# Optimization experiments

Measured on AMD Instinct MI355X. Metric: run time of the kernel, lower is better.

The kernel has to match this reference:

```python
import jax, jax.numpy as jnp
import numpy as np

D = 256   # input_size
H = 512   # hidden_size
A = 4     # alpha_dim
K = 2 * A * A  # output values per input dim (binary=False -> 2 params)


def _masks():
    # MADE sequential-ordering masks, per DART.create_masks
    in_deg = np.arange(D)
    hid_deg = np.arange(H) % (D - 1)
    out_deg = np.arange(D) - 1  # arange(D) % D - 1
    m0 = (hid_deg[:, None] >= in_deg[None, :]).astype(np.float32)   # [H, D]
    mh = (hid_deg[:, None] >= hid_deg[None, :]).astype(np.float32)  # [H, H]
    ml = (out_deg[:, None] >= hid_deg[None, :]).astype(np.float32)  # [D, H]
    # repeat(1, K).view(-1, H): each output-dim row repeated K consecutive times
    ml = np.repeat(ml, K, axis=0)                                    # [D*K, H]
    return jnp.asarray(m0), jnp.asarray(mh), jnp.asarray(ml)


def setup_inputs() -> dict:
    key = jax.random.key(0)
    ks = jax.random.split(key, 10)
    B = 1024
    x = jax.random.normal(ks[0], (B, D), dtype=jnp.float32)
    def lin(k, out_dim, in_dim):
        s = 1.0 / np.sqrt(in_dim)
        kw, kb = jax.random.split(k)
        W = jax.random.uniform(kw, (out_dim, in_dim), jnp.float32, -s, s)
        b = jax.random.uniform(kb, (out_dim,), jnp.float32, -s, s)
        return W, b
    W0, b0 = lin(ks[1], H, D)
    W1, b1 = lin(ks[2], H, H)
    W2, b2 = lin(ks[3], H, H)
    Wout, bout = lin(ks[4], D * K, H)
    # unnormalized_log_p_alpha initialized to log(1/A)
    ulpa = jnp.full((1, D - 1, 1, A), -np.log(A), dtype=jnp.float32)
    return {"x": x, "W0": W0, "b0": b0, "W1": W1, "b1": b1,
            "W2": W2, "b2": b2, "Wout": Wout, "bout": bout, "ulpa": ulpa}


def reference(x, W0, b0, W1, b1, W2, b2, Wout, bout, ulpa):
    m0, mh, ml = _masks()
    B = x.shape[0]
    # masked MLP (MADE)
    h = jax.nn.relu(x @ (m0 * W0).T + b0)
    h = jax.nn.relu(h @ (mh * W1).T + b1)
    h = jax.nn.relu(h @ (mh * W2).T + b2)
    theta = (h @ (ml * Wout).T + bout).reshape(B, D, 2, A, A)
    mu = theta[:, :, 0]                      # [B, D, A, A]
    std = jnp.exp(theta[:, :, 1]) + 0.01     # [B, D, A, A]
    xe = x[:, :, None, None]
    # Normal log-prob
    log_px = -0.5 * jnp.square((xe - mu) / std) - jnp.log(std) - 0.5 * jnp.log(2.0 * jnp.pi)
    # normalized log p(alpha): [1, D-1, 1, A]
    lpa = jax.nn.log_softmax(ulpa, axis=-1)
    joint = log_px[:, :-1] + lpa             # [B, D-1, A, A]
    first = joint[:, 0, 0:1]                 # [B, 1, A]
    inner = jnp.swapaxes(joint[:, 1:], 0, 1)  # [D-2, B, A, A]
    # HMM-style forward recursion: stable log-domain chain matmul via scan
    def step(carry, m):
        # carry: [B, 1, A]; m: [B, A, A]
        new = jax.nn.logsumexp(carry[:, :, :, None] + m[:, None, :, :], axis=-2)
        return new, None
    carry, _ = jax.lax.scan(step, first, inner)
    last = log_px[:, -1, :, 0:1]             # [B, A, 1]
    log_p = jax.nn.logsumexp(carry[:, :, :, None] + last[:, None, :, :], axis=-2)  # [B,1,1]
    return log_p, theta
```

## Files before the change

### kernel.cpp

```cpp
#include <hip/hip_runtime.h>
#include <math.h>

#define Bsz 1024
#define Dd  256
#define Hh  512
#define NOUT 8192

typedef __attribute__((ext_vector_type(8))) short bf8_t;
typedef __attribute__((ext_vector_type(4))) float f4_t;

__device__ inline ushort f2b(float f) {
  union { float f; unsigned u; } c; c.f = f;
  unsigned r = c.u + 0x7fffu + ((c.u >> 16) & 1u);
  return (ushort)(r >> 16);
}

__device__ inline void async16(const ushort* g, ushort* l) {
  __builtin_amdgcn_global_load_lds((const __attribute__((address_space(1))) void*)g,
                                   (__attribute__((address_space(3))) void*)l, 16, 0, 0);
}

__device__ inline int mod255(int v) {
  if (v >= 510) return v - 510;
  if (v >= 255) return v - 255;
  return v;
}

__global__ __launch_bounds__(256) void prep(
    const float* __restrict__ x,  const float* __restrict__ W0,
    const float* __restrict__ W1, const float* __restrict__ W2,
    const float* __restrict__ Wout, const float* __restrict__ ulpa,
    ushort* __restrict__ xb, ushort* __restrict__ w0b, ushort* __restrict__ w1b,
    ushort* __restrict__ w2b, ushort* __restrict__ woutb,
    float* __restrict__ lpa)
{
  const int blk = blockIdx.x, tid = threadIdx.x;
  if (blk == 2496) {
    if (tid < Dd - 1) {
      float v0 = ulpa[tid * 4 + 0], v1 = ulpa[tid * 4 + 1];
      float v2 = ulpa[tid * 4 + 2], v3 = ulpa[tid * 4 + 3];
      float m = fmaxf(fmaxf(v0, v1), fmaxf(v2, v3));
      float s = __expf(v0 - m) + __expf(v1 - m) + __expf(v2 - m) + __expf(v3 - m);
      float l = m + __logf(s);
      lpa[tid * 4 + 0] = v0 - l;
      lpa[tid * 4 + 1] = v1 - l;
      lpa[tid * 4 + 2] = v2 - l;
      lpa[tid * 4 + 3] = v3 - l;
    }
    return;
  }
  const float* src; ushort* dst; int lb, mode;
  if (blk < 128)      { src = x;    dst = xb;    lb = blk;       mode = 0; }
  else if (blk < 192) { src = W0;   dst = w0b;   lb = blk - 128; mode = 1; }
  else if (blk < 320) { src = W1;   dst = w1b;   lb = blk - 192; mode = 2; }
  else if (blk < 448) { src = W2;   dst = w2b;   lb = blk - 320; mode = 2; }
  else                { src = Wout; dst = woutb; lb = blk - 448; mode = 3; }

  const int e = lb * 2048 + tid * 8;
  float4 v0 = *(const float4*)(src + e);
  float4 v1 = *(const float4*)(src + e + 4);
  float vv[8] = {v0.x, v0.y, v0.z, v0.w, v1.x, v1.y, v1.z, v1.w};
  ushort u[8];
  if (mode == 0) {
#pragma unroll
    for (int i = 0; i < 8; i++) u[i] = f2b(vv[i]);
  } else if (mode == 1) {
    int n = e >> 8, k0 = e & 255, nd = mod255(n);
#pragma unroll
    for (int i = 0; i < 8; i++) u[i] = (nd >= k0 + i) ? f2b(vv[i]) : (ushort)0;
  } else if (mode == 2) {
    int n = e >> 9, k0 = e & 511, nd = mod255(n);
#pragma unroll
    for (int i = 0; i < 8; i++) u[i] = (nd >= mod255(k0 + i)) ? f2b(vv[i]) : (ushort)0;
  } else {
    int n = e >> 9, k0 = e & 511, nd = (n >> 5) - 1;
#pragma unroll
    for (int i = 0; i < 8; i++) u[i] = (nd >= mod255(k0 + i)) ? f2b(vv[i]) : (ushort)0;
  }
  *(ushort4*)(dst + e)     = *(ushort4*)&u[0];
  *(ushort4*)(dst + e + 4) = *(ushort4*)&u[4];
}

template<int KD>
__global__ __launch_bounds__(256) void gemm_s(
    const ushort* __restrict__ A, const ushort* __restrict__ W,
    const float* __restrict__ bias, ushort* __restrict__ Ch)
{
  __shared__ ushort As[64 * 64];
  __shared__ ushort Bs[32 * 64];
  const int tid = threadIdx.x, lane = tid & 63, wave = tid >> 6;
  const int row0 = blockIdx.y * 64, col0 = blockIdx.x * 32;
  const int fm = lane & 15, qq = lane >> 4;
  const int srow = lane >> 3, qslot = lane & 7;

  f4_t acc[2];
  acc[0] = (f4_t){0.f, 0.f, 0.f, 0.f};
  acc[1] = (f4_t){0.f, 0.f, 0.f, 0.f};

  for (int kt = 0; kt < KD; kt += 64) {
#pragma unroll
    for (int a = 0; a < 2; a++) {
      int rb = wave * 16 + a * 8;
      int r = rb + srow;
      int q = (qslot - r) & 7;
      async16(A + (size_t)(row0 + r) * KD + kt + q * 8, &As[rb * 64]);
    }
    {
      int rb = wave * 8;
      int r = rb + srow;
      int q = (qslot - r) & 7;
      async16(W + (size_t)(col0 + r) * KD + kt + q * 8, &Bs[rb * 64]);
    }
    __syncthreads();
#pragma unroll
    for (int t = 0; t < 2; t++) {
      int ra = wave * 16 + fm;
      int slota = ((t * 4 + qq) + ra) & 7;
      bf8_t af = *(const bf8_t*)&As[ra * 64 + slota * 8];
#pragma unroll
      for (int j = 0; j < 2; j++) {
        int rb = j * 16 + fm;
        int slot = ((t * 4 + qq) + rb) & 7;
        bf8_t bf = *(const bf8_t*)&Bs[rb * 64 + slot * 8];
        acc[j] = __builtin_amdgcn_mfma_f32_16x16x32_bf16(af, bf, acc[j], 0, 0, 0);
      }
    }
    __syncthreads();
  }

#pragma unroll
  for (int j = 0; j < 2; j++) {
    int col = col0 + j * 16 + fm;
    float bv = bias[col];
    int rbase = row0 + wave * 16 + qq * 4;
#pragma unroll
    for (int r = 0; r < 4; r++) {
      float t = fmaxf(acc[j][r] + bv, 0.0f);
      Ch[(size_t)(rbase + r) * Hh + col] = f2b(t);
    }
  }
}

__global__ __launch_bounds__(256) void gemm_big(
    const ushort* __restrict__ A, const ushort* __restrict__ W,
    const float* __restrict__ bias, float* __restrict__ Cf,
    int M, int N, int Kd)
{
  __shared__ ushort As[128 * 64];
  __shared__ ushort Bs[128 * 64];
  const int tid = threadIdx.x, lane = tid & 63, wave = tid >> 6;
  const int waveM = wave >> 1, waveN = wave & 1;
  const int row0 = blockIdx.y * 128, col0 = blockIdx.x * 128;
  const int fm = lane & 15, qq = lane >> 4;
  const int srow = lane >> 3, qslot = lane & 7;

  f4_t acc[4][4];
#pragma unroll
  for (int i = 0; i < 4; i++)
#pragma unroll
    for (int j = 0; j < 4; j++) acc[i][j] = (f4_t){0.f, 0.f, 0.f, 0.f};

  for (int kt = 0; kt < Kd; kt += 64) {
#pragma unroll
    for (int p = 0; p < 4; p++) {
      int rb = p * 32 + wave * 8;
      int r = rb + srow;
      int q = (qslot - r) & 7;
      async16(A + (size_t)(row0 + r) * Kd + kt + q * 8, &As[rb * 64]);
    }
#pragma unroll
    for (int p = 0; p < 4; p++) {
      int rb = p * 32 + wave * 8;
      int r = rb + srow;
      int q = (qslot - r) & 7;
      async16(W + (size_t)(col0 + r) * Kd + kt + q * 8, &Bs[rb * 64]);
    }
    __syncthreads();
#pragma unroll
    for (int t = 0; t < 2; t++) {
      bf8_t af[4], bf[4];
#pragma unroll
      for (int i = 0; i < 4; i++) {
        int r = waveM * 64 + i * 16 + fm;
        int slot = ((t * 4 + qq) + r) & 7;
        af[i] = *(const bf8_t*)&As[r * 64 + slot * 8];
      }
#pragma unroll
      for (int j = 0; j < 4; j++) {
        int r = waveN * 64 + j * 16 + fm;
        int slot = ((t * 4 + qq) + r) & 7;
        bf[j] = *(const bf8_t*)&Bs[r * 64 + slot * 8];
      }
#pragma unroll
      for (int i = 0; i < 4; i++)
#pragma unroll
        for (int j = 0; j < 4; j++)
          acc[i][j] = __builtin_amdgcn_mfma_f32_16x16x32_bf16(af[i], bf[j], acc[i][j], 0, 0, 0);
    }
    __syncthreads();
  }

#pragma unroll
  for (int j = 0; j < 4; j++) {
    int col = col0 + waveN * 64 + j * 16 + fm;
    float bv = bias[col];
#pragma unroll
    for (int i = 0; i < 4; i++) {
      int rbase = row0 + waveM * 64 + i * 16 + qq * 4;
#pragma unroll
      for (int r = 0; r < 4; r++)
        Cf[(size_t)(rbase + r) * N + col] = acc[i][j][r] + bv;
    }
  }
}

__global__ __launch_bounds__(256) void chain2(
    const float* __restrict__ x, const float* __restrict__ theta,
    const float* __restrict__ lpa, float* __restrict__ logp)
{
  const int b = blockIdx.x;
  const int tid = threadIdx.x;
  const int seg = tid >> 4, e = tid & 15;
  const int i = e >> 2, jj = e & 3;
  const int base = (tid & 63) & ~15;
  const float C0 = 0.91893853320467274178f;
  const float* th = theta + (size_t)b * NOUT;
  const float* xb = x + (size_t)b * Dd;
  __shared__ float Ts[16][16];

  const int d0 = 1 + seg * 16;
  const int d1 = min(d0 + 16, Dd - 1);

  auto stepm = [&](int d) -> float {
    float mu = th[d * 32 + e];
    float ls = th[d * 32 + 16 + e];
    float s  = __expf(ls) + 0.01f;
    float z  = (xb[d] - mu) * __builtin_amdgcn_rcpf(s);
    return -0.5f * z * z - __logf(s) - C0 + lpa[d * 4 + jj];
  };

  float T = stepm(d0);
  for (int d = d0 + 1; d < d1; d++) {
    float m_ = stepm(d);
    float v0 = __shfl(T, base + i * 4 + 0) + __shfl(m_, base + 0 * 4 + jj);
    float v1 = __shfl(T, base + i * 4 + 1) + __shfl(m_, base + 1 * 4 + jj);
    float v2 = __shfl(T, base + i * 4 + 2) + __shfl(m_, base + 2 * 4 + jj);
    float v3 = __shfl(T, base + i * 4 + 3) + __shfl(m_, base + 3 * 4 + jj);
    float mx = fmaxf(fmaxf(v0, v1), fmaxf(v2, v3));
    float s  = __expf(v0 - mx) + __expf(v1 - mx) + __expf(v2 - mx) + __expf(v3 - mx);
    T = mx + __logf(s);
  }
  Ts[seg][e] = T;
  __syncthreads();

  if (tid < 4) {
    const int j = tid;
    float mu = th[j], ls = th[16 + j];
    float s = __expf(ls) + 0.01f;
    float z = (xb[0] - mu) * __builtin_amdgcn_rcpf(s);
    float carry = -0.5f * z * z - __logf(s) - C0 + lpa[j];
#pragma unroll 1
    for (int sg = 0; sg < 16; sg++) {
      float c0 = __shfl(carry, 0);
      float c1 = __shfl(carry, 1);
      float c2 = __shfl(carry, 2);
      float c3 = __shfl(carry, 3);
      float v0 = c0 + Ts[sg][0 * 4 + j];
      float v1 = c1 + Ts[sg][1 * 4 + j];
      float v2 = c2 + Ts[sg][2 * 4 + j];
      float v3 = c3 + Ts[sg][3 * 4 + j];
      float mx = fmaxf(fmaxf(v0, v1), fmaxf(v2, v3));
      float ss = __expf(v0 - mx) + __expf(v1 - mx) + __expf(v2 - mx) + __expf(v3 - mx);
      carry = mx + __logf(ss);
    }
    float mu2 = th[255 * 32 + j * 4], ls2 = th[255 * 32 + 16 + j * 4];
    float s2 = __expf(ls2) + 0.01f;
    float z2 = (xb[255] - mu2) * __builtin_amdgcn_rcpf(s2);
    float v = carry - 0.5f * z2 * z2 - __logf(s2) - C0;
    float mx = fmaxf(v, __shfl_xor(v, 1));
    mx = fmaxf(mx, __shfl_xor(mx, 2));
    float ee = __expf(v - mx);
    ee += __shfl_xor(ee, 1);
    ee += __shfl_xor(ee, 2);
    if (j == 0) logp[b] = mx + __logf(ee);
  }
}

extern "C" void kernel_launch(void* const* d_in, const int* in_sizes, int n_in,
                              void* d_out, int out_size, void* d_ws, size_t ws_size,
                              hipStream_t stream)
{
  const float* x    = (const float*)d_in[0];
  const float* W0   = (const float*)d_in[1];
  const float* b0   = (const float*)d_in[2];
  const float* W1   = (const float*)d_in[3];
  const float* b1   = (const float*)d_in[4];
  const float* W2   = (const float*)d_in[5];
  const float* b2   = (const float*)d_in[6];
  const float* Wout = (const float*)d_in[7];
  const float* bout = (const float*)d_in[8];
  const float* ulpa = (const float*)d_in[9];

  float* out   = (float*)d_out;
  float* logp  = out;
  float* theta = out + Bsz;

  ushort* ws    = (ushort*)d_ws;
  ushort* xb    = ws;
  ushort* w0b   = xb + 262144;
  ushort* w1b   = w0b + 131072;
  ushort* w2b   = w1b + 262144;
  ushort* woutb = w2b + 262144;
  ushort* h0    = woutb + 4194304;
  ushort* h1    = h0 + 524288;
  ushort* h2    = h1 + 524288;
  float*  lpa   = (float*)(h2 + 524288);

  prep<<<2497, 256, 0, stream>>>(x, W0, W1, W2, Wout, ulpa,
                                 xb, w0b, w1b, w2b, woutb, lpa);
  gemm_s<Dd><<<dim3(16, 16), 256, 0, stream>>>(xb, w0b, b0, h0);
  gemm_s<Hh><<<dim3(16, 16), 256, 0, stream>>>(h0, w1b, b1, h1);
  gemm_s<Hh><<<dim3(16, 16), 256, 0, stream>>>(h1, w2b, b2, h2);
  gemm_big<<<dim3(NOUT / 128, Bsz / 128), 256, 0, stream>>>(h2, woutb, bout, theta, Bsz, NOUT, Hh);
  chain2<<<Bsz, 256, 0, stream>>>(x, theta, lpa, logp);
}
```

Before: 139.5 us.

## Multi-buffer GEMM tile loads and parallelize chain reduction with a tree

The small GEMMs now use a triple-buffered LDS pipeline and the output GEMM a double-buffered one. Async global-to-LDS loads for the next tiles are issued before computing the current tile, with explicit vmcnt waits and barriers in place of __syncthreads. The chain kernel moves to 512 threads: it stages each row's theta, x and log p(alpha) into padded shared memory, runs shorter 8-step segments, and combines the 32 segment matrices with a log-depth tree of log-semiring matrix products instead of a serial 16-step loop. The GEMM changes aim to hide global load latency at the cost of more LDS per block, and the chain changes aim to shorten its serial dependency chain.

```diff
diff --git a/kernel.cpp b/kernel.cpp
--- a/kernel.cpp
+++ b/kernel.cpp
@@ -86,8 +86,9 @@
     const ushort* __restrict__ A, const ushort* __restrict__ W,
     const float* __restrict__ bias, ushort* __restrict__ Ch)
 {
-  __shared__ ushort As[64 * 64];
-  __shared__ ushort Bs[32 * 64];
+  constexpr int NT = KD / 64;
+  __shared__ ushort As[3][64 * 64];
+  __shared__ ushort Bs[3][32 * 64];
   const int tid = threadIdx.x, lane = tid & 63, wave = tid >> 6;
   const int row0 = blockIdx.y * 64, col0 = blockIdx.x * 32;
   const int fm = lane & 15, qq = lane >> 4;
@@ -97,35 +98,47 @@
   acc[0] = (f4_t){0.f, 0.f, 0.f, 0.f};
   acc[1] = (f4_t){0.f, 0.f, 0.f, 0.f};
 
-  for (int kt = 0; kt < KD; kt += 64) {
+  auto stage = [&](int buf, int kt) {
 #pragma unroll
     for (int a = 0; a < 2; a++) {
       int rb = wave * 16 + a * 8;
       int r = rb + srow;
       int q = (qslot - r) & 7;
-      async16(A + (size_t)(row0 + r) * KD + kt + q * 8, &As[rb * 64]);
+      async16(A + (size_t)(row0 + r) * KD + kt + q * 8, &As[buf][rb * 64]);
     }
     {
       int rb = wave * 8;
       int r = rb + srow;
       int q = (qslot - r) & 7;
-      async16(W + (size_t)(col0 + r) * KD + kt + q * 8, &Bs[rb * 64]);
-    }
-    __syncthreads();
+      async16(W + (size_t)(col0 + r) * KD + kt + q * 8, &Bs[buf][rb * 64]);
+    }
+  };
+
+  stage(0, 0);
+  stage(1, 64);
+
+#pragma unroll
+  for (int i = 0; i < NT; i++) {
+    if (i + 1 < NT) asm volatile("s_waitcnt vmcnt(3)" ::: "memory");
+    else            asm volatile("s_waitcnt vmcnt(0)" ::: "memory");
+    __builtin_amdgcn_s_barrier();
+    asm volatile("" ::: "memory");
+    if (i + 2 < NT) stage((i + 2) % 3, (i + 2) * 64);
+    const int buf = i % 3;
 #pragma unroll
     for (int t = 0; t < 2; t++) {
       int ra = wave * 16 + fm;
       int slota = ((t * 4 + qq) + ra) & 7;
-      bf8_t af = *(const bf8_t*)&As[ra * 64 + slota * 8];
+      bf8_t af = *(const bf8_t*)&As[buf][ra * 64 + slota * 8];
 #pragma unroll
       for (int j = 0; j < 2; j++) {
         int rb = j * 16 + fm;
         int slot = ((t * 4 + qq) + rb) & 7;
-        bf8_t bf = *(const bf8_t*)&Bs[rb * 64 + slot * 8];
+        bf8_t bf = *(const bf8_t*)&Bs[buf][rb * 64 + slot * 8];
         acc[j] = __builtin_amdgcn_mfma_f32_16x16x32_bf16(af, bf, acc[j], 0, 0, 0);
       }
     }
-    __syncthreads();
+    asm volatile("s_waitcnt lgkmcnt(0)" ::: "memory");
   }
 
 #pragma unroll
@@ -146,8 +159,8 @@
     const float* __restrict__ bias, float* __restrict__ Cf,
     int M, int N, int Kd)
 {
-  __shared__ ushort As[128 * 64];
-  __shared__ ushort Bs[128 * 64];
+  __shared__ ushort As[2][128 * 64];
+  __shared__ ushort Bs[2][128 * 64];
   const int tid = threadIdx.x, lane = tid & 63, wave = tid >> 6;
   const int waveM = wave >> 1, waveN = wave & 1;
   const int row0 = blockIdx.y * 128, col0 = blockIdx.x * 128;
@@ -160,22 +173,30 @@
 #pragma unroll
     for (int j = 0; j < 4; j++) acc[i][j] = (f4_t){0.f, 0.f, 0.f, 0.f};
 
-  for (int kt = 0; kt < Kd; kt += 64) {
+  auto stage = [&](int buf, int kt) {
 #pragma unroll
     for (int p = 0; p < 4; p++) {
       int rb = p * 32 + wave * 8;
       int r = rb + srow;
       int q = (qslot - r) & 7;
-      async16(A + (size_t)(row0 + r) * Kd + kt + q * 8, &As[rb * 64]);
+      async16(A + (size_t)(row0 + r) * Kd + kt + q * 8, &As[buf][rb * 64]);
     }
 #pragma unroll
     for (int p = 0; p < 4; p++) {
       int rb = p * 32 + wave * 8;
       int r = rb + srow;
       int q = (qslot - r) & 7;
-      async16(W + (size_t)(col0 + r) * Kd + kt + q * 8, &Bs[rb * 64]);
-    }
-    __syncthreads();
+      async16(W + (size_t)(col0 + r) * Kd + kt + q * 8, &Bs[buf][rb * 64]);
+    }
+  };
+
+  stage(0, 0);
+  int cur = 0;
+  for (int kt = 0; kt < Kd; kt += 64) {
+    asm volatile("s_waitcnt vmcnt(0)" ::: "memory");
+    __builtin_amdgcn_s_barrier();
+    asm volatile("" ::: "memory");
+    if (kt + 64 < Kd) stage(cur ^ 1, kt + 64);
 #pragma unroll
     for (int t = 0; t < 2; t++) {
       bf8_t af[4], bf[4];
@@ -183,13 +204,13 @@
       for (int i = 0; i < 4; i++) {
         int r = waveM * 64 + i * 16 + fm;
         int slot = ((t * 4 + qq) + r) & 7;
-        af[i] = *(const bf8_t*)&As[r * 64 + slot * 8];
+        af[i] = *(const bf8_t*)&As[cur][r * 64 + slot * 8];
       }
 #pragma unroll
       for (int j = 0; j < 4; j++) {
         int r = waveN * 64 + j * 16 + fm;
         int slot = ((t * 4 + qq) + r) & 7;
-        bf[j] = *(const bf8_t*)&Bs[r * 64 + slot * 8];
+        bf[j] = *(const bf8_t*)&Bs[cur][r * 64 + slot * 8];
       }
 #pragma unroll
       for (int i = 0; i < 4; i++)
@@ -197,7 +218,8 @@
         for (int j = 0; j < 4; j++)
           acc[i][j] = __builtin_amdgcn_mfma_f32_16x16x32_bf16(af[i], bf[j], acc[i][j], 0, 0, 0);
     }
-    __syncthreads();
+    asm volatile("s_waitcnt lgkmcnt(0)" ::: "memory");
+    cur ^= 1;
   }
 
 #pragma unroll
@@ -214,75 +236,106 @@
   }
 }
 
-__global__ __launch_bounds__(256) void chain2(
+__global__ __launch_bounds__(512) void chain2(
     const float* __restrict__ x, const float* __restrict__ theta,
     const float* __restrict__ lpa, float* __restrict__ logp)
 {
+  __shared__ float ths[256 * 33];
+  __shared__ float xs[256];
+  __shared__ float lps[255 * 5];
+  __shared__ float TA[32][16];
+  __shared__ float TB[16][16];
+
   const int b = blockIdx.x;
   const int tid = threadIdx.x;
-  const int seg = tid >> 4, e = tid & 15;
-  const int i = e >> 2, jj = e & 3;
+  const float C0 = 0.91893853320467274178f;
+
+  const float4* src = (const float4*)(theta + (size_t)b * NOUT);
+#pragma unroll
+  for (int it = 0; it < 4; it++) {
+    int t = tid + it * 512;
+    float4 v = src[t];
+    int d = t >> 3, c = (t & 7) * 4;
+    float* p = &ths[d * 33 + c];
+    p[0] = v.x; p[1] = v.y; p[2] = v.z; p[3] = v.w;
+  }
+  if (tid < 64) ((float4*)xs)[tid] = ((const float4*)(x + (size_t)b * Dd))[tid];
+  if (tid < 255) {
+    float4 v = ((const float4*)lpa)[tid];
+    float* p = &lps[tid * 5];
+    p[0] = v.x; p[1] = v.y; p[2] = v.z; p[3] = v.w;
+  }
+  __syncthreads();
+
+  const int seg = tid >> 4, e = tid & 15, ii = e >> 2, jj = e & 3;
   const int base = (tid & 63) & ~15;
-  const float C0 = 0.91893853320467274178f;
-  const float* th = theta + (size_t)b * NOUT;
-  const float* xb = x + (size_t)b * Dd;
-  __shared__ float Ts[16][16];
-
-  const int d0 = 1 + seg * 16;
-  const int d1 = min(d0 + 16, Dd - 1);
+  const int d0 = 1 + seg * 8;
+  const int d1 = min(d0 + 8, Dd - 1);
 
   auto stepm = [&](int d) -> float {
-    float mu = th[d * 32 + e];
-    float ls = th[d * 32 + 16 + e];
+    float mu = ths[d * 33 + e];
+    float ls = ths[d * 33 + 16 + e];
     float s  = __expf(ls) + 0.01f;
-    float z  = (xb[d] - mu) * __builtin_amdgcn_rcpf(s);
-    return -0.5f * z * z - __logf(s) - C0 + lpa[d * 4 + jj];
+    float z  = (xs[d] - mu) * __builtin_amdgcn_rcpf(s);
+    return -0.5f * z * z - __logf(s) - C0 + lps[d * 5 + jj];
   };
 
   float T = stepm(d0);
   for (int d = d0 + 1; d < d1; d++) {
     float m_ = stepm(d);
-    float v0 = __shfl(T, base + i * 4 + 0) + __shfl(m_, base + 0 * 4 + jj);
-    float v1 = __shfl(T, base + i * 4 + 1) + __shfl(m_, base + 1 * 4 + jj);
-    float v2 = __shfl(T, base + i * 4 + 2) + __shfl(m_, base + 2 * 4 + jj);
-    float v3 = __shfl(T, base + i * 4 + 3) + __shfl(m_, base + 3 * 4 + jj);
+    float v0 = __shfl(T, base + ii * 4 + 0) + __shfl(m_, base + 0 * 4 + jj);
+    float v1 = __shfl(T, base + ii * 4 + 1) + __shfl(m_, base + 1 * 4 + jj);
+    float v2 = __shfl(T, base + ii * 4 + 2) + __shfl(m_, base + 2 * 4 + jj);
+    float v3 = __shfl(T, base + ii * 4 + 3) + __shfl(m_, base + 3 * 4 + jj);
     float mx = fmaxf(fmaxf(v0, v1), fmaxf(v2, v3));
     float s  = __expf(v0 - mx) + __expf(v1 - mx) + __expf(v2 - mx) + __expf(v3 - mx);
     T = mx + __logf(s);
   }
-  Ts[seg][e] = T;
+  TA[seg][e] = T;
   __syncthreads();
 
-  if (tid < 4) {
-    const int j = tid;
-    float mu = th[j], ls = th[16 + j];
-    float s = __expf(ls) + 0.01f;
-    float z = (xb[0] - mu) * __builtin_amdgcn_rcpf(s);
-    float carry = -0.5f * z * z - __logf(s) - C0 + lpa[j];
-#pragma unroll 1
-    for (int sg = 0; sg < 16; sg++) {
-      float c0 = __shfl(carry, 0);
-      float c1 = __shfl(carry, 1);
-      float c2 = __shfl(carry, 2);
-      float c3 = __shfl(carry, 3);
-      float v0 = c0 + Ts[sg][0 * 4 + j];
-      float v1 = c1 + Ts[sg][1 * 4 + j];
-      float v2 = c2 + Ts[sg][2 * 4 + j];
-      float v3 = c3 + Ts[sg][3 * 4 + j];
+  float (*cur)[16] = TA;
+  float (*nxt)[16] = TB;
+#pragma unroll
+  for (int n = 16; n >= 1; n >>= 1) {
+    if (tid < n * 16) {
+      int p = tid >> 4, ee = tid & 15, i2 = ee >> 2, j2 = ee & 3;
+      const float* L = cur[2 * p];
+      const float* R = cur[2 * p + 1];
+      float v0 = L[i2 * 4 + 0] + R[0 * 4 + j2];
+      float v1 = L[i2 * 4 + 1] + R[1 * 4 + j2];
+      float v2 = L[i2 * 4 + 2] + R[2 * 4 + j2];
+      float v3 = L[i2 * 4 + 3] + R[3 * 4 + j2];
       float mx = fmaxf(fmaxf(v0, v1), fmaxf(v2, v3));
       float ss = __expf(v0 - mx) + __expf(v1 - mx) + __expf(v2 - mx) + __expf(v3 - mx);
-      carry = mx + __logf(ss);
-    }
-    float mu2 = th[255 * 32 + j * 4], ls2 = th[255 * 32 + 16 + j * 4];
-    float s2 = __expf(ls2) + 0.01f;
-    float z2 = (xb[255] - mu2) * __builtin_amdgcn_rcpf(s2);
-    float v = carry - 0.5f * z2 * z2 - __logf(s2) - C0;
+      nxt[p][ee] = mx + __logf(ss);
+    }
+    __syncthreads();
+    float (*tmp)[16] = cur; cur = nxt; nxt = tmp;
+  }
+
+  if (tid < 16) {
+    int i = tid >> 2, j = tid & 3;
+    float mu0 = ths[i], ls0 = ths[16 + i];
+    float s0 = __expf(ls0) + 0.01f;
+    float z0 = (xs[0] - mu0) * __builtin_amdgcn_rcpf(s0);
+    float c0 = -0.5f * z0 * z0 - __logf(s0) - C0 + lps[i];
+    float muL = ths[255 * 33 + j * 4];
+    float lsL = ths[255 * 33 + 16 + j * 4];
+    float sL = __expf(lsL) + 0.01f;
+    float zL = (xs[255] - muL) * __builtin_amdgcn_rcpf(sL);
+    float lL = -0.5f * zL * zL - __logf(sL) - C0;
+    float v = c0 + cur[0][tid] + lL;
     float mx = fmaxf(v, __shfl_xor(v, 1));
     mx = fmaxf(mx, __shfl_xor(mx, 2));
+    mx = fmaxf(mx, __shfl_xor(mx, 4));
+    mx = fmaxf(mx, __shfl_xor(mx, 8));
     float ee = __expf(v - mx);
     ee += __shfl_xor(ee, 1);
     ee += __shfl_xor(ee, 2);
-    if (j == 0) logp[b] = mx + __logf(ee);
+    ee += __shfl_xor(ee, 4);
+    ee += __shfl_xor(ee, 8);
+    if (tid == 0) logp[b] = mx + __logf(ee);
   }
 }
 
@@ -322,5 +375,5 @@
   gemm_s<Hh><<<dim3(16, 16), 256, 0, stream>>>(h0, w1b, b1, h1);
   gemm_s<Hh><<<dim3(16, 16), 256, 0, stream>>>(h1, w2b, b2, h2);
   gemm_big<<<dim3(NOUT / 128, Bsz / 128), 256, 0, stream>>>(h2, woutb, bout, theta, Bsz, NOUT, Hh);
-  chain2<<<Bsz, 256, 0, stream>>>(x, theta, lpa, logp);
-}
+  chain2<<<Bsz, 512, 0, stream>>>(x, theta, lpa, logp);
+}
```

Result: faster. 136.1 us (-2.4%).
